# Kernel tuning notes

Measured on AMD Instinct MI355X. Metric: run time of the kernel, lower is better.

## Reference

```python
import jax, jax.numpy as jnp
import numpy as np

B, C, H, W = 1, 192, 96, 96


def setup_inputs() -> dict:
    key = jax.random.key(0)
    k1, k2 = jax.random.split(key, 2)
    latent_feats = jax.random.normal(k1, (B, C, H, W), dtype=jnp.float32)
    refined_feats = jax.random.normal(k2, (B, C, H, W), dtype=jnp.float32)
    w_4 = jnp.ones((1, C, H, W), dtype=jnp.float32)
    w_5 = jnp.ones((1, C, H, W), dtype=jnp.float32)
    return {"latent_feats": latent_feats, "refined_feats": refined_feats, "w_4": w_4, "w_5": w_5}


def reference(latent_feats, refined_feats, w_4, w_5):
    # b == 1 (torch.mm requires 2D operands, so the original only works for batch 1)
    hw = H * W
    lat = (latent_feats * w_4)[0].reshape(C, hw)          # [c, hw]
    ref = refined_feats[0].reshape(C, hw)                 # [c, hw]
    scores = jnp.einsum('cn,cm->nm', ref, lat)            # [(hw)_ref, (hw)_lat]
    attn = jax.nn.softmax(scores, axis=-2)                # softmax over rows (dim -2)
    ctx = jnp.einsum('cn,nm->cm', lat, attn)              # [c, hw]
    return refined_feats * w_5 + ctx.reshape(1, C, H, W)
```

## Files before the change

### kernel.cpp

```cpp
#include <hip/hip_runtime.h>
#include <stdint.h>


#define NQ 9216
#define NC 192
#define FR 1769472
#define LOG2E 1.4426950408889634f
#define M0L 36.06737602f

typedef short    bfrag  __attribute__((ext_vector_type(8)));
typedef _Float16 hfrag  __attribute__((ext_vector_type(8)));
typedef short    sfrag4 __attribute__((ext_vector_type(4)));
typedef float    facc16 __attribute__((ext_vector_type(16)));
typedef int      ifrag4 __attribute__((ext_vector_type(4)));

__device__ __forceinline__ short f2bf(float x) {
    uint32_t u = __builtin_bit_cast(uint32_t, x);
    u = (u + 0x7fffu + ((u >> 16) & 1u)) >> 16;
    return (short)u;
}
__device__ __forceinline__ float bf2f(short s) {
    uint32_t u = ((uint32_t)(uint16_t)s) << 16;
    return __builtin_bit_cast(float, u);
}
__device__ __forceinline__ int cvtpk_bf16(float lo, float hi) {
    int r;
    asm("v_cvt_pk_bf16_f32 %0, %1, %2" : "=v"(r) : "v"(lo), "v"(hi));
    return r;
}
__device__ __forceinline__ float exp2_raw(float x) {
    float r;
    asm("v_exp_f32 %0, %1" : "=v"(r) : "v"(x));
    return r;
}
__device__ __forceinline__ void gload_lds16(const void* g, void* l) {
    __builtin_amdgcn_global_load_lds(
        (__attribute__((address_space(1))) const void*)(uintptr_t)g,
        (__attribute__((address_space(3))) void*)(uint32_t)(uintptr_t)l,
        16, 0, 0);
}

__global__ __launch_bounds__(256) void InterGate_prep(
    const float* __restrict__ latent, const float* __restrict__ refined,
    const float* __restrict__ w4,
    short* __restrict__ Qf, short* __restrict__ KV)
{
    const int wid  = blockIdx.x * 4 + (threadIdx.x >> 6);
    const int lane = threadIdx.x & 63;
    const int l32  = lane & 31, h = lane >> 5;

    if (wid < 3456) {
        const int qw = wid / 12, t = wid % 12;
        const int q  = qw * 32 + l32;
        const int c0 = t * 16 + h * 8;
        hfrag hv;
        #pragma unroll
        for (int i = 0; i < 8; i++) {
            size_t idx = (size_t)(c0 + i) * NQ + q;
            hv[i] = (_Float16)(latent[idx] * w4[idx] * LOG2E);
        }
        *(hfrag*)(void*)(Qf + ((size_t)wid * 64 + lane) * 8) = hv;
    } else if (wid < 6912) {
        const int u = wid - 3456;
        const int g = u / 12, t = u % 12;
        const int key = g * 32 + l32;
        const int c0  = t * 16 + h * 8;
        hfrag hv;
        #pragma unroll
        for (int i = 0; i < 8; i++) {
            size_t idx = (size_t)(c0 + i) * NQ + key;
            hv[i] = (_Float16)refined[idx];
        }
        *(hfrag*)(void*)(KV + (size_t)g * 12288 + ((t * 64 + lane) * 8)) = hv;
    } else {
        const int u = wid - 6912;
        const int g = u / 12, r = u % 12;
        const int T = r / 6, cb = r % 6;
        const int c  = cb * 32 + l32;
        const int k0 = g * 32 + T * 16 + 4 * h;
        bfrag bv;
        #pragma unroll
        for (int i = 0; i < 8; i++) {
            const int row = k0 + (i & 3) + 8 * (i >> 2);
            size_t idx = (size_t)c * NQ + row;
            bv[i] = f2bf(latent[idx] * w4[idx]);
        }
        *(bfrag*)(void*)(KV + (size_t)g * 12288 + 6144 + ((T * 6 + cb) * 64 + lane) * 8) = bv;
    }
}

__device__ __forceinline__ void stage24(const short* KVsrc, char* dstb,
                                        int w, int lane) {
    const char* src = (const char*)KVsrc + w * 6144 + lane * 16;
    char* dst = dstb + w * 6144;
    #pragma unroll
    for (int j = 0; j < 6; j++) gload_lds16(src + j * 1024, dst + j * 1024);
}

#define KLD(n)  *(const hfrag*)(const void*)(kb + (n) * 512 + lane * 8)
#define VLD(n)  *(const bfrag*)(const void*)(kb + 6144 + (n) * 512 + lane * 8)
#define QKM(kf, t)  S = __builtin_amdgcn_mfma_f32_32x32x16_f16((kf), qf[t], S, 0, 0, 0)
#define PVM(vf, cb, pf) O[cb] = __builtin_amdgcn_mfma_f32_32x32x16_bf16((vf), (pf), O[cb], 0, 0, 0)

__global__ __launch_bounds__(256, 2) void InterGate_flash(
    const short* __restrict__ Qf, const short* __restrict__ KV,
    short* __restrict__ Opart, float* __restrict__ l_ws, int KS)
{
    __shared__ __align__(16) short kv[3][12288];

    const int tid  = threadIdx.x;
    const int lane = tid & 63, w = tid >> 6;
    const int l32  = lane & 31, h = lane >> 5;
    const int qt   = blockIdx.x, ks = blockIdx.y;

    const int base = 288 / KS, rem = 288 % KS;
    const int start = ks * base + (ks < rem ? ks : rem);
    const int cnt   = base + (ks < rem ? 1 : 0);

    const int qw = qt * 4 + w;
    hfrag qf[12];
    #pragma unroll
    for (int t = 0; t < 12; t++)
        qf[t] = *(const hfrag*)(const void*)(Qf + (((size_t)qw * 12 + t) * 64 + lane) * 8);

    facc16 O[6];
    #pragma unroll
    for (int cb = 0; cb < 6; cb++)
        #pragma unroll
        for (int j = 0; j < 16; j++) O[cb][j] = 0.f;
    float lsum = 0.f;

    stage24(KV + (size_t)start * 12288,       (char*)&kv[0][0], w, lane);
    if (cnt > 1)
        stage24(KV + (size_t)(start + 1) * 12288, (char*)&kv[1][0], w, lane);

    const short* b0 = &kv[0][0];
    const short* b1 = &kv[1][0];
    const short* b2 = &kv[2][0];

    for (int kt = 0; kt < cnt; kt++) {
        if (kt + 1 < cnt) { asm volatile("s_waitcnt vmcnt(6)" ::: "memory"); }
        else              { asm volatile("s_waitcnt vmcnt(0)" ::: "memory"); }
        __builtin_amdgcn_s_barrier();

        if (kt + 2 < cnt)
            stage24(KV + (size_t)(start + kt + 2) * 12288, (char*)b2, w, lane);

        const short* kb = b0;

        hfrag k0 = KLD(0), k1 = KLD(1), k2 = KLD(2), k3 = KLD(3);
        hfrag k4 = KLD(4), k5 = KLD(5), k6 = KLD(6), k7 = KLD(7);
        facc16 S;
        #pragma unroll
        for (int j = 0; j < 16; j++) S[j] = 0.f;
        __builtin_amdgcn_s_setprio(1);
        QKM(k0, 0); QKM(k1, 1); QKM(k2, 2); QKM(k3, 3);
        hfrag k8 = KLD(8), k9 = KLD(9), k10 = KLD(10), k11 = KLD(11);
        QKM(k4, 4); QKM(k5, 5); QKM(k6, 6); QKM(k7, 7);
        bfrag v0 = VLD(0), v1 = VLD(1), v2 = VLD(2), v3 = VLD(3);
        QKM(k8, 8); QKM(k9, 9); QKM(k10, 10); QKM(k11, 11);
        __builtin_amdgcn_s_setprio(0);

        float p[16];
        #pragma unroll
        for (int j = 0; j < 16; j++) p[j] = exp2_raw(S[j] - M0L);
        lsum += (((p[0]+p[1])+(p[2]+p[3]))+((p[4]+p[5])+(p[6]+p[7])))
              + (((p[8]+p[9])+(p[10]+p[11]))+((p[12]+p[13])+(p[14]+p[15])));
        int cp[8];
        #pragma unroll
        for (int a = 0; a < 8; a++) cp[a] = cvtpk_bf16(p[2 * a], p[2 * a + 1]);
        bfrag pf0 = __builtin_bit_cast(bfrag, (ifrag4){cp[0], cp[1], cp[2], cp[3]});
        bfrag pf1 = __builtin_bit_cast(bfrag, (ifrag4){cp[4], cp[5], cp[6], cp[7]});

        bfrag v4 = VLD(4), v5 = VLD(5), v6 = VLD(6), v7 = VLD(7);
        __builtin_amdgcn_s_setprio(1);
        PVM(v0, 0, pf0); PVM(v1, 1, pf0); PVM(v2, 2, pf0); PVM(v3, 3, pf0);
        bfrag v8 = VLD(8), v9 = VLD(9), v10 = VLD(10), v11 = VLD(11);
        PVM(v4, 4, pf0); PVM(v5, 5, pf0);
        PVM(v6, 0, pf1); PVM(v7, 1, pf1);
        PVM(v8, 2, pf1); PVM(v9, 3, pf1); PVM(v10, 4, pf1); PVM(v11, 5, pf1);
        __builtin_amdgcn_s_setprio(0);

        const short* tmp = b0; b0 = b1; b1 = b2; b2 = tmp;
    }

    const int q0 = qt * 128 + w * 32 + l32;
    short* row = Opart + ((size_t)ks * NQ + q0) * NC;
    #pragma unroll
    for (int cb = 0; cb < 6; cb++) {
        #pragma unroll
        for (int g = 0; g < 4; g++) {
            const int c0 = cb * 32 + 8 * g + 4 * h;
            sfrag4 s4;
            #pragma unroll
            for (int r = 0; r < 4; r++) s4[r] = f2bf(O[cb][4 * g + r]);
            *(sfrag4*)(void*)(row + c0) = s4;
        }
    }
    float lt = lsum + __shfl_xor(lsum, 32);
    if (h == 0) l_ws[(size_t)ks * NQ + q0] = lt;
}

__global__ __launch_bounds__(256) void InterGate_combine(
    const short* __restrict__ Opart, const float* __restrict__ l_ws,
    const float* __restrict__ refined, const float* __restrict__ w5,
    float* __restrict__ out, int KS)
{
    __shared__ float ctx[32][193];
    __shared__ float sInv[32];
    const int qt = blockIdx.x, tid = threadIdx.x;

    if (tid < 32) {
        const int q = qt * 32 + tid;
        float L = 0.f;
        for (int ks = 0; ks < KS; ks++) L += l_ws[(size_t)ks * NQ + q];
        sInv[tid] = 1.f / L;
    }
    __syncthreads();

    for (int u = tid; u < 768; u += 256) {
        const int ql = u / 24, c0 = (u % 24) * 8;
        float acc[8] = {0.f, 0.f, 0.f, 0.f, 0.f, 0.f, 0.f, 0.f};
        for (int ks = 0; ks < KS; ks++) {
            bfrag pk = *(const bfrag*)(const void*)&Opart[((size_t)ks * NQ + qt * 32 + ql) * NC + c0];
            #pragma unroll
            for (int j = 0; j < 8; j++) acc[j] += bf2f(pk[j]);
        }
        const float inv = sInv[ql];
        #pragma unroll
        for (int j = 0; j < 8; j++) ctx[ql][c0 + j] = acc[j] * inv;
    }
    __syncthreads();

    for (int u = tid; u < 6144; u += 256) {
        const int c = u / 32, qx = u % 32;
        size_t o = (size_t)c * NQ + qt * 32 + qx;
        out[o] = refined[o] * w5[o] + ctx[qx][c];
    }
}

extern "C" void kernel_launch(void* const* d_in, const int* in_sizes, int n_in,
                              void* d_out, int out_size, void* d_ws, size_t ws_size,
                              hipStream_t stream)
{
    (void)in_sizes; (void)n_in; (void)out_size;
    const float* latent  = (const float*)d_in[0];
    const float* refined = (const float*)d_in[1];
    const float* w4      = (const float*)d_in[2];
    const float* w5      = (const float*)d_in[3];
    float* out = (float*)d_out;

    short* Qf = (short*)d_ws;
    short* KV = Qf + FR;
    const size_t basebytes = (size_t)3 * FR * 2;

    const int opts[4] = {7, 4, 2, 1};
    int KS = 0;
    for (int i = 0; i < 4; i++) {
        size_t need = basebytes + (size_t)opts[i] * ((size_t)NQ * NC * 2 + (size_t)NQ * 4);
        if (need <= ws_size) { KS = opts[i]; break; }
    }
    if (KS == 0) return;

    short* Opart = (short*)((char*)d_ws + basebytes);
    float* l_ws  = (float*)((char*)d_ws + basebytes + (size_t)KS * NQ * NC * 2);

    InterGate_prep<<<2592, 256, 0, stream>>>(latent, refined, w4, Qf, KV);
    dim3 fg(72, KS);
    InterGate_flash<<<fg, 256, 0, stream>>>(Qf, KV, Opart, l_ws, KS);
    InterGate_combine<<<288, 256, 0, stream>>>(Opart, l_ws, refined, w5, out, KS);
}
```

Baseline: 98.06 us.

## Process two query tiles per wave to reuse K/V fragments across MFMAs

Flash kernel now launches 128 threads (2 waves) per block, and each wave handles two 32-row query tiles. Every K and V fragment read from LDS therefore feeds two MFMAs, halving LDS reads per MFMA. Each wave now stages 12 KV loads instead of 6. The row-max offset is folded into the accumulator init, and sched_group_barriers interleave LDS reads with MFMAs. In exchange, register pressure roughly doubles (launch bounds drop to 1 block) and fewer waves are resident to hide latency.

```diff
diff --git a/kernel.cpp b/kernel.cpp
--- a/kernel.cpp
+++ b/kernel.cpp
@@ -91,18 +91,23 @@
 
 __device__ __forceinline__ void stage24(const short* KVsrc, char* dstb,
                                         int w, int lane) {
-    const char* src = (const char*)KVsrc + w * 6144 + lane * 16;
-    char* dst = dstb + w * 6144;
+    const char* src = (const char*)KVsrc + w * 12288 + lane * 16;
+    char* dst = dstb + w * 12288;
     #pragma unroll
-    for (int j = 0; j < 6; j++) gload_lds16(src + j * 1024, dst + j * 1024);
+    for (int j = 0; j < 12; j++) gload_lds16(src + j * 1024, dst + j * 1024);
 }
 
 #define KLD(n)  *(const hfrag*)(const void*)(kb + (n) * 512 + lane * 8)
 #define VLD(n)  *(const bfrag*)(const void*)(kb + 6144 + (n) * 512 + lane * 8)
-#define QKM(kf, t)  S = __builtin_amdgcn_mfma_f32_32x32x16_f16((kf), qf[t], S, 0, 0, 0)
-#define PVM(vf, cb, pf) O[cb] = __builtin_amdgcn_mfma_f32_32x32x16_bf16((vf), (pf), O[cb], 0, 0, 0)
-
-__global__ __launch_bounds__(256, 2) void InterGate_flash(
+#define QK2(kf, t) do { \
+    S0 = __builtin_amdgcn_mfma_f32_32x32x16_f16((kf), qa[t], S0, 0, 0, 0); \
+    S1 = __builtin_amdgcn_mfma_f32_32x32x16_f16((kf), qb[t], S1, 0, 0, 0); } while (0)
+#define PV2(vf, cb, pA, pB) do { \
+    OA[cb] = __builtin_amdgcn_mfma_f32_32x32x16_bf16((vf), (pA), OA[cb], 0, 0, 0); \
+    OB[cb] = __builtin_amdgcn_mfma_f32_32x32x16_bf16((vf), (pB), OB[cb], 0, 0, 0); } while (0)
+#define SGB __builtin_amdgcn_sched_group_barrier
+
+__global__ __launch_bounds__(128, 1) void InterGate_flash(
     const short* __restrict__ Qf, const short* __restrict__ KV,
     short* __restrict__ Opart, float* __restrict__ l_ws, int KS)
 {
@@ -117,18 +122,21 @@
     const int start = ks * base + (ks < rem ? ks : rem);
     const int cnt   = base + (ks < rem ? 1 : 0);
 
-    const int qw = qt * 4 + w;
-    hfrag qf[12];
+    const int qwA = qt * 4 + w * 2;
+    hfrag qa[12], qb[12];
     #pragma unroll
-    for (int t = 0; t < 12; t++)
-        qf[t] = *(const hfrag*)(const void*)(Qf + (((size_t)qw * 12 + t) * 64 + lane) * 8);
-
-    facc16 O[6];
+    for (int t = 0; t < 12; t++) {
+        qa[t] = *(const hfrag*)(const void*)(Qf + (((size_t)qwA * 12 + t) * 64 + lane) * 8);
+        qb[t] = *(const hfrag*)(const void*)(Qf + (((size_t)(qwA + 1) * 12 + t) * 64 + lane) * 8);
+    }
+
+    facc16 OA[6], OB[6];
     #pragma unroll
-    for (int cb = 0; cb < 6; cb++)
-        #pragma unroll
-        for (int j = 0; j < 16; j++) O[cb][j] = 0.f;
-    float lsum = 0.f;
+    for (int cb = 0; cb < 6; cb++) {
+        #pragma unroll
+        for (int j = 0; j < 16; j++) { OA[cb][j] = 0.f; OB[cb][j] = 0.f; }
+    }
+    float lsA = 0.f, lsB = 0.f;
 
     stage24(KV + (size_t)start * 12288,       (char*)&kv[0][0], w, lane);
     if (cnt > 1)
@@ -139,7 +147,7 @@
     const short* b2 = &kv[2][0];
 
     for (int kt = 0; kt < cnt; kt++) {
-        if (kt + 1 < cnt) { asm volatile("s_waitcnt vmcnt(6)" ::: "memory"); }
+        if (kt + 1 < cnt) { asm volatile("s_waitcnt vmcnt(12)" ::: "memory"); }
         else              { asm volatile("s_waitcnt vmcnt(0)" ::: "memory"); }
         __builtin_amdgcn_s_barrier();
 
@@ -149,56 +157,91 @@
         const short* kb = b0;
 
         hfrag k0 = KLD(0), k1 = KLD(1), k2 = KLD(2), k3 = KLD(3);
-        hfrag k4 = KLD(4), k5 = KLD(5), k6 = KLD(6), k7 = KLD(7);
-        facc16 S;
-        #pragma unroll
-        for (int j = 0; j < 16; j++) S[j] = 0.f;
+        facc16 S0, S1;
+        #pragma unroll
+        for (int j = 0; j < 16; j++) { S0[j] = -M0L; S1[j] = -M0L; }
         __builtin_amdgcn_s_setprio(1);
-        QKM(k0, 0); QKM(k1, 1); QKM(k2, 2); QKM(k3, 3);
-        hfrag k8 = KLD(8), k9 = KLD(9), k10 = KLD(10), k11 = KLD(11);
-        QKM(k4, 4); QKM(k5, 5); QKM(k6, 6); QKM(k7, 7);
-        bfrag v0 = VLD(0), v1 = VLD(1), v2 = VLD(2), v3 = VLD(3);
-        QKM(k8, 8); QKM(k9, 9); QKM(k10, 10); QKM(k11, 11);
+        hfrag k4  = KLD(4);  QK2(k0, 0);
+        hfrag k5  = KLD(5);  QK2(k1, 1);
+        hfrag k6  = KLD(6);  QK2(k2, 2);
+        hfrag k7  = KLD(7);  QK2(k3, 3);
+        hfrag k8  = KLD(8);  QK2(k4, 4);
+        hfrag k9  = KLD(9);  QK2(k5, 5);
+        hfrag k10 = KLD(10); QK2(k6, 6);
+        hfrag k11 = KLD(11); QK2(k7, 7);
+        bfrag v0  = VLD(0);  QK2(k8, 8);
+        bfrag v1  = VLD(1);  QK2(k9, 9);
+        bfrag v2  = VLD(2);  QK2(k10, 10);
+        bfrag v3  = VLD(3);  QK2(k11, 11);
         __builtin_amdgcn_s_setprio(0);
 
-        float p[16];
-        #pragma unroll
-        for (int j = 0; j < 16; j++) p[j] = exp2_raw(S[j] - M0L);
-        lsum += (((p[0]+p[1])+(p[2]+p[3]))+((p[4]+p[5])+(p[6]+p[7])))
-              + (((p[8]+p[9])+(p[10]+p[11]))+((p[12]+p[13])+(p[14]+p[15])));
-        int cp[8];
-        #pragma unroll
-        for (int a = 0; a < 8; a++) cp[a] = cvtpk_bf16(p[2 * a], p[2 * a + 1]);
-        bfrag pf0 = __builtin_bit_cast(bfrag, (ifrag4){cp[0], cp[1], cp[2], cp[3]});
-        bfrag pf1 = __builtin_bit_cast(bfrag, (ifrag4){cp[4], cp[5], cp[6], cp[7]});
-
-        bfrag v4 = VLD(4), v5 = VLD(5), v6 = VLD(6), v7 = VLD(7);
+        float pA[16], pB[16];
+        #pragma unroll
+        for (int j = 0; j < 16; j++) {
+            pA[j] = exp2_raw(S0[j]);
+            pB[j] = exp2_raw(S1[j]);
+        }
+        lsA += (((pA[0]+pA[1])+(pA[2]+pA[3]))+((pA[4]+pA[5])+(pA[6]+pA[7])))
+             + (((pA[8]+pA[9])+(pA[10]+pA[11]))+((pA[12]+pA[13])+(pA[14]+pA[15])));
+        lsB += (((pB[0]+pB[1])+(pB[2]+pB[3]))+((pB[4]+pB[5])+(pB[6]+pB[7])))
+             + (((pB[8]+pB[9])+(pB[10]+pB[11]))+((pB[12]+pB[13])+(pB[14]+pB[15])));
+        int cpA[8], cpB[8];
+        #pragma unroll
+        for (int a = 0; a < 8; a++) {
+            cpA[a] = cvtpk_bf16(pA[2 * a], pA[2 * a + 1]);
+            cpB[a] = cvtpk_bf16(pB[2 * a], pB[2 * a + 1]);
+        }
+        bfrag pfA0 = __builtin_bit_cast(bfrag, (ifrag4){cpA[0], cpA[1], cpA[2], cpA[3]});
+        bfrag pfA1 = __builtin_bit_cast(bfrag, (ifrag4){cpA[4], cpA[5], cpA[6], cpA[7]});
+        bfrag pfB0 = __builtin_bit_cast(bfrag, (ifrag4){cpB[0], cpB[1], cpB[2], cpB[3]});
+        bfrag pfB1 = __builtin_bit_cast(bfrag, (ifrag4){cpB[4], cpB[5], cpB[6], cpB[7]});
+
         __builtin_amdgcn_s_setprio(1);
-        PVM(v0, 0, pf0); PVM(v1, 1, pf0); PVM(v2, 2, pf0); PVM(v3, 3, pf0);
-        bfrag v8 = VLD(8), v9 = VLD(9), v10 = VLD(10), v11 = VLD(11);
-        PVM(v4, 4, pf0); PVM(v5, 5, pf0);
-        PVM(v6, 0, pf1); PVM(v7, 1, pf1);
-        PVM(v8, 2, pf1); PVM(v9, 3, pf1); PVM(v10, 4, pf1); PVM(v11, 5, pf1);
+        bfrag v4  = VLD(4);  PV2(v0, 0, pfA0, pfB0);
+        bfrag v5  = VLD(5);  PV2(v1, 1, pfA0, pfB0);
+        bfrag v6  = VLD(6);  PV2(v2, 2, pfA0, pfB0);
+        bfrag v7  = VLD(7);  PV2(v3, 3, pfA0, pfB0);
+        bfrag v8  = VLD(8);  PV2(v4, 4, pfA0, pfB0);
+        bfrag v9  = VLD(9);  PV2(v5, 5, pfA0, pfB0);
+        bfrag v10 = VLD(10); PV2(v6, 0, pfA1, pfB1);
+        bfrag v11 = VLD(11); PV2(v7, 1, pfA1, pfB1);
+        PV2(v8, 2, pfA1, pfB1);  PV2(v9, 3, pfA1, pfB1);
+        PV2(v10, 4, pfA1, pfB1); PV2(v11, 5, pfA1, pfB1);
         __builtin_amdgcn_s_setprio(0);
 
+        SGB(0x100, 4, 0);
+        #pragma unroll
+        for (int i = 0; i < 12; i++) { SGB(0x100, 1, 0); SGB(0x8, 2, 0); }
+        #pragma unroll
+        for (int i = 0; i < 8; i++)  { SGB(0x100, 1, 0); SGB(0x8, 3, 0); }
+
         const short* tmp = b0; b0 = b1; b1 = b2; b2 = tmp;
     }
 
-    const int q0 = qt * 128 + w * 32 + l32;
-    short* row = Opart + ((size_t)ks * NQ + q0) * NC;
+    const int q0 = qt * 128 + w * 64 + l32;
+    short* rowA = Opart + ((size_t)ks * NQ + q0) * NC;
+    short* rowB = rowA + (size_t)32 * NC;
     #pragma unroll
     for (int cb = 0; cb < 6; cb++) {
         #pragma unroll
         for (int g = 0; g < 4; g++) {
             const int c0 = cb * 32 + 8 * g + 4 * h;
-            sfrag4 s4;
+            sfrag4 sa, sb;
             #pragma unroll
-            for (int r = 0; r < 4; r++) s4[r] = f2bf(O[cb][4 * g + r]);
-            *(sfrag4*)(void*)(row + c0) = s4;
-        }
-    }
-    float lt = lsum + __shfl_xor(lsum, 32);
-    if (h == 0) l_ws[(size_t)ks * NQ + q0] = lt;
+            for (int r = 0; r < 4; r++) {
+                sa[r] = f2bf(OA[cb][4 * g + r]);
+                sb[r] = f2bf(OB[cb][4 * g + r]);
+            }
+            *(sfrag4*)(void*)(rowA + c0) = sa;
+            *(sfrag4*)(void*)(rowB + c0) = sb;
+        }
+    }
+    float la = lsA + __shfl_xor(lsA, 32);
+    float lb = lsB + __shfl_xor(lsB, 32);
+    if (h == 0) {
+        l_ws[(size_t)ks * NQ + q0]      = la;
+        l_ws[(size_t)ks * NQ + q0 + 32] = lb;
+    }
 }
 
 __global__ __launch_bounds__(256) void InterGate_combine(
@@ -267,6 +310,6 @@
 
     InterGate_prep<<<2592, 256, 0, stream>>>(latent, refined, w4, Qf, KV);
     dim3 fg(72, KS);
-    InterGate_flash<<<fg, 256, 0, stream>>>(Qf, KV, Opart, l_ws, KS);
+    InterGate_flash<<<fg, 128, 0, stream>>>(Qf, KV, Opart, l_ws, KS);
     InterGate_combine<<<288, 256, 0, stream>>>(Opart, l_ws, refined, w5, out, KS);
 }
```

Measured after the change: 102.1 us. +4.1%, slower.

## Restructure flash kernel into 8-wave blocks with 64-key phased double buffering

Applied to the files above, without the earlier changes.

Doubles the workgroup to 512 threads (8 waves, 256 queries per block) and processes two 32-key sub-tiles per iteration, with LDS double buffering of 48KB tiles. Global-to-LDS loads for the next tile are split into chunks and issued between four compute phases separated by barriers. The softmax offset is folded into the accumulator initialisation. The aim is more key/value reuse per LDS load and finer interleaving of loads with MFMA work. In exchange it adds many more barriers per iteration and launches half as many blocks, which may reduce occupancy or parallelism.

```diff
diff --git a/kernel.cpp b/kernel.cpp
--- a/kernel.cpp
+++ b/kernel.cpp
@@ -89,7 +89,7 @@
     }
 }
 
-__device__ __forceinline__ void stage24(const short* KVsrc, char* dstb,
+__device__ __forceinline__ void stage48(const short* KVsrc, char* dstb,
                                         int w, int lane) {
     const char* src = (const char*)KVsrc + w * 6144 + lane * 16;
     char* dst = dstb + w * 6144;
@@ -97,27 +97,50 @@
     for (int j = 0; j < 6; j++) gload_lds16(src + j * 1024, dst + j * 1024);
 }
 
-#define KLD(n)  *(const hfrag*)(const void*)(kb + (n) * 512 + lane * 8)
-#define VLD(n)  *(const bfrag*)(const void*)(kb + 6144 + (n) * 512 + lane * 8)
-#define QKM(kf, t)  S = __builtin_amdgcn_mfma_f32_32x32x16_f16((kf), qf[t], S, 0, 0, 0)
+#define KLD(base, n)  *(const hfrag*)(const void*)(kb + (base) + (n) * 512 + lane * 8)
+#define VLD(base, n)  *(const bfrag*)(const void*)(kb + (base) + (n) * 512 + lane * 8)
+#define SOFTMAX(Sx, pf0, pf1) do {                                            \
+    float p_[16];                                                             \
+    _Pragma("unroll")                                                         \
+    for (int j = 0; j < 16; j++) p_[j] = exp2_raw((Sx)[j]);                   \
+    lsum += (((p_[0]+p_[1])+(p_[2]+p_[3]))+((p_[4]+p_[5])+(p_[6]+p_[7])))     \
+          + (((p_[8]+p_[9])+(p_[10]+p_[11]))+((p_[12]+p_[13])+(p_[14]+p_[15])));\
+    int cp_[8];                                                               \
+    _Pragma("unroll")                                                         \
+    for (int a = 0; a < 8; a++) cp_[a] = cvtpk_bf16(p_[2*a], p_[2*a+1]);      \
+    pf0 = __builtin_bit_cast(bfrag, (ifrag4){cp_[0], cp_[1], cp_[2], cp_[3]});\
+    pf1 = __builtin_bit_cast(bfrag, (ifrag4){cp_[4], cp_[5], cp_[6], cp_[7]});\
+} while (0)
+#define PHASE_WAIT do {                                                       \
+    __builtin_amdgcn_s_barrier();                                             \
+    asm volatile("s_waitcnt lgkmcnt(0)" ::: "memory");                        \
+    __builtin_amdgcn_sched_barrier(0);                                        \
+} while (0)
+#define GLD2(jj) do { if (kt + 1 < cnt) {                                     \
+    const char* s_ = (const char*)(KV + (size_t)(start + kt + 1) * 24576)     \
+                     + w * 6144 + (jj) * 2048 + lane * 16;                    \
+    char* d_ = (char*)b1 + w * 6144 + (jj) * 2048;                            \
+    gload_lds16(s_, d_); gload_lds16(s_ + 1024, d_ + 1024);                   \
+} } while (0)
+#define QKM(Sx, kf, t) Sx = __builtin_amdgcn_mfma_f32_32x32x16_f16((kf), qf[t], Sx, 0, 0, 0)
 #define PVM(vf, cb, pf) O[cb] = __builtin_amdgcn_mfma_f32_32x32x16_bf16((vf), (pf), O[cb], 0, 0, 0)
 
-__global__ __launch_bounds__(256, 2) void InterGate_flash(
+__global__ __launch_bounds__(512, 2) void InterGate_flash(
     const short* __restrict__ Qf, const short* __restrict__ KV,
     short* __restrict__ Opart, float* __restrict__ l_ws, int KS)
 {
-    __shared__ __align__(16) short kv[3][12288];
+    __shared__ __align__(16) short kv[2][24576];
 
     const int tid  = threadIdx.x;
     const int lane = tid & 63, w = tid >> 6;
     const int l32  = lane & 31, h = lane >> 5;
     const int qt   = blockIdx.x, ks = blockIdx.y;
 
-    const int base = 288 / KS, rem = 288 % KS;
+    const int base = 144 / KS, rem = 144 % KS;
     const int start = ks * base + (ks < rem ? ks : rem);
     const int cnt   = base + (ks < rem ? 1 : 0);
 
-    const int qw = qt * 4 + w;
+    const int qw = qt * 8 + w;
     hfrag qf[12];
     #pragma unroll
     for (int t = 0; t < 12; t++)
@@ -130,61 +153,71 @@
         for (int j = 0; j < 16; j++) O[cb][j] = 0.f;
     float lsum = 0.f;
 
-    stage24(KV + (size_t)start * 12288,       (char*)&kv[0][0], w, lane);
-    if (cnt > 1)
-        stage24(KV + (size_t)(start + 1) * 12288, (char*)&kv[1][0], w, lane);
+    stage48(KV + (size_t)start * 24576, (char*)&kv[0][0], w, lane);
 
     const short* b0 = &kv[0][0];
     const short* b1 = &kv[1][0];
-    const short* b2 = &kv[2][0];
 
     for (int kt = 0; kt < cnt; kt++) {
-        if (kt + 1 < cnt) { asm volatile("s_waitcnt vmcnt(6)" ::: "memory"); }
-        else              { asm volatile("s_waitcnt vmcnt(0)" ::: "memory"); }
+        asm volatile("s_waitcnt vmcnt(0)" ::: "memory");
         __builtin_amdgcn_s_barrier();
-
-        if (kt + 2 < cnt)
-            stage24(KV + (size_t)(start + kt + 2) * 12288, (char*)b2, w, lane);
-
         const short* kb = b0;
 
-        hfrag k0 = KLD(0), k1 = KLD(1), k2 = KLD(2), k3 = KLD(3);
-        hfrag k4 = KLD(4), k5 = KLD(5), k6 = KLD(6), k7 = KLD(7);
-        facc16 S;
-        #pragma unroll
-        for (int j = 0; j < 16; j++) S[j] = 0.f;
+        hfrag k0 = KLD(0,0), k1 = KLD(0,1), k2 = KLD(0,2), k3 = KLD(0,3);
+        hfrag k4 = KLD(0,4), k5 = KLD(0,5), k6 = KLD(0,6), k7 = KLD(0,7);
+        GLD2(0);
+        facc16 S0, S1;
+        #pragma unroll
+        for (int j = 0; j < 16; j++) { S0[j] = -M0L; S1[j] = -M0L; }
+        PHASE_WAIT;
         __builtin_amdgcn_s_setprio(1);
-        QKM(k0, 0); QKM(k1, 1); QKM(k2, 2); QKM(k3, 3);
-        hfrag k8 = KLD(8), k9 = KLD(9), k10 = KLD(10), k11 = KLD(11);
-        QKM(k4, 4); QKM(k5, 5); QKM(k6, 6); QKM(k7, 7);
-        bfrag v0 = VLD(0), v1 = VLD(1), v2 = VLD(2), v3 = VLD(3);
-        QKM(k8, 8); QKM(k9, 9); QKM(k10, 10); QKM(k11, 11);
+        QKM(S0, k0, 0); QKM(S0, k1, 1); QKM(S0, k2, 2); QKM(S0, k3, 3);
+        hfrag k8 = KLD(0,8), k9 = KLD(0,9), k10 = KLD(0,10), k11 = KLD(0,11);
+        QKM(S0, k4, 4); QKM(S0, k5, 5); QKM(S0, k6, 6); QKM(S0, k7, 7);
+        QKM(S0, k8, 8); QKM(S0, k9, 9); QKM(S0, k10, 10); QKM(S0, k11, 11);
         __builtin_amdgcn_s_setprio(0);
 
-        float p[16];
-        #pragma unroll
-        for (int j = 0; j < 16; j++) p[j] = exp2_raw(S[j] - M0L);
-        lsum += (((p[0]+p[1])+(p[2]+p[3]))+((p[4]+p[5])+(p[6]+p[7])))
-              + (((p[8]+p[9])+(p[10]+p[11]))+((p[12]+p[13])+(p[14]+p[15])));
-        int cp[8];
-        #pragma unroll
-        for (int a = 0; a < 8; a++) cp[a] = cvtpk_bf16(p[2 * a], p[2 * a + 1]);
-        bfrag pf0 = __builtin_bit_cast(bfrag, (ifrag4){cp[0], cp[1], cp[2], cp[3]});
-        bfrag pf1 = __builtin_bit_cast(bfrag, (ifrag4){cp[4], cp[5], cp[6], cp[7]});
-
-        bfrag v4 = VLD(4), v5 = VLD(5), v6 = VLD(6), v7 = VLD(7);
+        k0 = KLD(12288,0); k1 = KLD(12288,1); k2 = KLD(12288,2); k3 = KLD(12288,3);
+        k4 = KLD(12288,4); k5 = KLD(12288,5); k6 = KLD(12288,6); k7 = KLD(12288,7);
+        GLD2(1);
+        PHASE_WAIT;
+        __builtin_amdgcn_s_setprio(1);
+        QKM(S1, k0, 0); QKM(S1, k1, 1); QKM(S1, k2, 2); QKM(S1, k3, 3);
+        k8 = KLD(12288,8); k9 = KLD(12288,9); k10 = KLD(12288,10); k11 = KLD(12288,11);
+        QKM(S1, k4, 4); QKM(S1, k5, 5); QKM(S1, k6, 6); QKM(S1, k7, 7);
+        QKM(S1, k8, 8); QKM(S1, k9, 9); QKM(S1, k10, 10); QKM(S1, k11, 11);
+        __builtin_amdgcn_s_setprio(0);
+
+        bfrag pf0, pf1;
+        SOFTMAX(S0, pf0, pf1);
+        bfrag v0 = VLD(6144,0), v1 = VLD(6144,1), v2 = VLD(6144,2), v3 = VLD(6144,3);
+        bfrag v4 = VLD(6144,4), v5 = VLD(6144,5), v6 = VLD(6144,6), v7 = VLD(6144,7);
+        GLD2(2);
+        PHASE_WAIT;
         __builtin_amdgcn_s_setprio(1);
         PVM(v0, 0, pf0); PVM(v1, 1, pf0); PVM(v2, 2, pf0); PVM(v3, 3, pf0);
-        bfrag v8 = VLD(8), v9 = VLD(9), v10 = VLD(10), v11 = VLD(11);
+        bfrag v8 = VLD(6144,8), v9 = VLD(6144,9), v10 = VLD(6144,10), v11 = VLD(6144,11);
         PVM(v4, 4, pf0); PVM(v5, 5, pf0);
         PVM(v6, 0, pf1); PVM(v7, 1, pf1);
         PVM(v8, 2, pf1); PVM(v9, 3, pf1); PVM(v10, 4, pf1); PVM(v11, 5, pf1);
         __builtin_amdgcn_s_setprio(0);
 
-        const short* tmp = b0; b0 = b1; b1 = b2; b2 = tmp;
-    }
-
-    const int q0 = qt * 128 + w * 32 + l32;
+        SOFTMAX(S1, pf0, pf1);
+        v0 = VLD(18432,0); v1 = VLD(18432,1); v2 = VLD(18432,2); v3 = VLD(18432,3);
+        v4 = VLD(18432,4); v5 = VLD(18432,5); v6 = VLD(18432,6); v7 = VLD(18432,7);
+        PHASE_WAIT;
+        __builtin_amdgcn_s_setprio(1);
+        PVM(v0, 0, pf0); PVM(v1, 1, pf0); PVM(v2, 2, pf0); PVM(v3, 3, pf0);
+        v8 = VLD(18432,8); v9 = VLD(18432,9); v10 = VLD(18432,10); v11 = VLD(18432,11);
+        PVM(v4, 4, pf0); PVM(v5, 5, pf0);
+        PVM(v6, 0, pf1); PVM(v7, 1, pf1);
+        PVM(v8, 2, pf1); PVM(v9, 3, pf1); PVM(v10, 4, pf1); PVM(v11, 5, pf1);
+        __builtin_amdgcn_s_setprio(0);
+
+        const short* tmp = b0; b0 = b1; b1 = tmp;
+    }
+
+    const int q0 = qt * 256 + w * 32 + l32;
     short* row = Opart + ((size_t)ks * NQ + q0) * NC;
     #pragma unroll
     for (int cb = 0; cb < 6; cb++) {
@@ -266,7 +299,7 @@
     float* l_ws  = (float*)((char*)d_ws + basebytes + (size_t)KS * NQ * NC * 2);
 
     InterGate_prep<<<2592, 256, 0, stream>>>(latent, refined, w4, Qf, KV);
-    dim3 fg(72, KS);
-    InterGate_flash<<<fg, 256, 0, stream>>>(Qf, KV, Opart, l_ws, KS);
+    dim3 fg(36, KS);
+    InterGate_flash<<<fg, 512, 0, stream>>>(Qf, KV, Opart, l_ws, KS);
     InterGate_combine<<<288, 256, 0, stream>>>(Opart, l_ws, refined, w5, out, KS);
 }
```

After: 92.14 us. 6.0% less time.
